# Kernel optimization log

Hardware: AMD Instinct MI355X
Metric: run time of the kernel (lower is better)

The kernel has to match this reference:

```python
import jax, jax.numpy as jnp
import numpy as np

N_NODES = 500_000
N_EDGES = 16_000_000
N_LAYERS = 49
ALPHA = 0.3  # GCN2Conv alpha; beta = 1.0 (no theta/layer given)

# per-layer activation applied AFTER the conv (layer index 0-based)
_LEAKY = {1, 11, 21, 31, 41}
_SIG = {4, 14, 24, 34, 44}


def setup_inputs() -> dict:
    key = jax.random.key(0)
    k1, k2, k3 = jax.random.split(key, 3)
    x = jax.random.normal(k1, (N_NODES, 1), dtype=jnp.float32)
    adj = jax.random.randint(k2, (2, N_EDGES), 0, N_NODES, dtype=jnp.int64)
    # 49 scalar (1x1) layer weights
    w = jax.random.normal(k3, (N_LAYERS,), dtype=jnp.float32) * 0.1
    return {"input": x, "w": w, "adj": adj}


def _gcn_norm(adj, n):
    # add self-loops, symmetric normalization D^-1/2 (A+I) D^-1/2
    loops = jnp.arange(n, dtype=adj.dtype)
    src = jnp.concatenate([adj[0], loops])
    dst = jnp.concatenate([adj[1], loops])
    deg = jax.ops.segment_sum(jnp.ones(src.shape[0], jnp.float32), dst, num_segments=n)
    dis = 1.0 / jnp.sqrt(deg)  # deg >= 1 due to self-loops
    ew = dis[src] * dis[dst]
    return src, dst, ew


def reference(input, w, adj):
    n = input.shape[0]
    x0 = input.astype(jnp.float32)
    src, dst, ew = _gcn_norm(adj, n)
    ewc = ew[:, None]  # [E+N, 1]

    def gcn2(x, wl):
        h = jax.ops.segment_sum(ewc * x[src], dst, num_segments=n)  # A_hat @ x
        comb = (1.0 - ALPHA) * h + ALPHA * x0                       # residual mix
        return comb * wl                                            # 1x1 weight, beta=1

    x = x0
    for i in range(N_LAYERS):
        y = gcn2(x, w[i])
        if i == 0:
            x = y  # no activation after gcn1
        elif i == N_LAYERS - 1:
            x = n * jax.nn.sigmoid(y)  # CustomSigmoid: len(x) * sigmoid(x)
        elif i in _LEAKY:
            x = jax.nn.leaky_relu(y, 0.01)
        elif i in _SIG:
            x = jax.nn.sigmoid(y)
        else:
            x = jax.nn.relu(y)
        # dropout(p=0.0) is identity
    return jnp.squeeze(x, 1).astype(jnp.int64)
```

## Files before the change

kernel.cpp:

```cpp
#include <hip/hip_runtime.h>
#include <math.h>

#define NN 500000
#define NE 16000000
#define NBKT 1954
#define PB 16384
#define NPB_BLOCKS ((NE + PB - 1) / PB)
#define BKT_CAP 9216

__global__ __launch_bounds__(256) void hist_kernel(const int4* __restrict__ dst4,
                                                   int* __restrict__ bcnt) {
    __shared__ int lh[NBKT];
    for (int i = threadIdx.x; i < NBKT; i += 256) lh[i] = 0;
    __syncthreads();
    long base4 = (long)blockIdx.x * (PB / 4);
    for (int k = 0; k < PB / 4; k += 256) {
        long i4 = base4 + k + threadIdx.x;
        if (i4 < NE / 4) {
            int4 d = dst4[i4];
            atomicAdd(&lh[d.x >> 8], 1);
            atomicAdd(&lh[d.y >> 8], 1);
            atomicAdd(&lh[d.z >> 8], 1);
            atomicAdd(&lh[d.w >> 8], 1);
        }
    }
    __syncthreads();
    for (int i = threadIdx.x; i < NBKT; i += 256) {
        int c = lh[i];
        if (c) atomicAdd(&bcnt[i], c);
    }
}

__global__ __launch_bounds__(256) void scan_buckets(int* __restrict__ bcnt,
                                                    int* __restrict__ bbase) {
    __shared__ int sh[256];
    __shared__ int carry_sh;
    if (threadIdx.x == 0) carry_sh = 0;
    __syncthreads();
    for (int base = 0; base < NBKT; base += 256) {
        int i = base + threadIdx.x;
        int v = (i < NBKT) ? bcnt[i] : 0;
        sh[threadIdx.x] = v;
        __syncthreads();
        for (int off = 1; off < 256; off <<= 1) {
            int t = (threadIdx.x >= off) ? sh[threadIdx.x - off] : 0;
            __syncthreads();
            sh[threadIdx.x] += t;
            __syncthreads();
        }
        int incl = sh[threadIdx.x];
        int c = carry_sh;
        __syncthreads();
        if (i < NBKT) {
            int ex = c + incl - v;
            bbase[i] = ex;
            bcnt[i] = ex;
        }
        if (threadIdx.x == 255) carry_sh = c + incl;
        __syncthreads();
    }
    if (threadIdx.x == 0) bbase[NBKT] = NE;
}

__global__ __launch_bounds__(256) void partition_kernel(const int* __restrict__ src,
                                                        const int* __restrict__ dst,
                                                        int* __restrict__ bcur,
                                                        int* __restrict__ ebuf) {
    __shared__ int lh[NBKT];
    for (int i = threadIdx.x; i < NBKT; i += 256) lh[i] = 0;
    __syncthreads();
    long base = (long)blockIdx.x * PB;
    for (int k = 0; k < PB; k += 256) {
        long e = base + k + threadIdx.x;
        if (e < NE) atomicAdd(&lh[dst[e] >> 8], 1);
    }
    __syncthreads();
    for (int i = threadIdx.x; i < NBKT; i += 256) {
        int c = lh[i];
        if (c) lh[i] = atomicAdd(&bcur[i], c);
    }
    __syncthreads();
    for (int k = 0; k < PB; k += 256) {
        long e = base + k + threadIdx.x;
        if (e < NE) {
            int d = dst[e];
            int pos = atomicAdd(&lh[d >> 8], 1);
            ebuf[pos] = ((d & 255) << 19) | src[e];
        }
    }
}

__global__ __launch_bounds__(256) void bucket_csr(const int* __restrict__ bbase,
                                                  int* __restrict__ ebuf,
                                                  int* __restrict__ rp,
                                                  float* __restrict__ dis) {
    __shared__ int eds[BKT_CAP];
    __shared__ int cnt[256];
    __shared__ int scn[256];
    int b = blockIdx.x;
    int ebase = bbase[b];
    int nb = bbase[b + 1] - ebase;
    if (nb > BKT_CAP) nb = BKT_CAP;
    for (int i = threadIdx.x; i < nb; i += 256) eds[i] = ebuf[ebase + i];
    cnt[threadIdx.x] = 0;
    __syncthreads();
    for (int i = threadIdx.x; i < nb; i += 256) atomicAdd(&cnt[eds[i] >> 19], 1);
    __syncthreads();
    int my = cnt[threadIdx.x];
    scn[threadIdx.x] = my;
    __syncthreads();
    for (int off = 1; off < 256; off <<= 1) {
        int t = (threadIdx.x >= off) ? scn[threadIdx.x - off] : 0;
        __syncthreads();
        scn[threadIdx.x] += t;
        __syncthreads();
    }
    int excl = scn[threadIdx.x] - my;
    int v = b * 256 + threadIdx.x;
    if (v < NN) {
        rp[v] = ebase + excl;
        dis[v] = rsqrtf((float)(my + 1));
    }
    __syncthreads();
    cnt[threadIdx.x] = excl;
    __syncthreads();
    for (int i = threadIdx.x; i < nb; i += 256) {
        int p = eds[i];
        int pos = atomicAdd(&cnt[p >> 19], 1);
        ebuf[ebase + pos] = p & 0x7FFFF;
    }
    if (b == 0 && threadIdx.x == 0) rp[NN] = NE;
}

__global__ void init_z(const float* __restrict__ x0, const float* __restrict__ dis,
                       float* __restrict__ z) {
    int i = blockIdx.x * 256 + threadIdx.x;
    if (i < NN) z[i] = x0[i] * dis[i];
}

__global__ __launch_bounds__(256) void layer_kernel(
        const int* __restrict__ rp, const int* __restrict__ csr,
        const float* __restrict__ zin, const float* __restrict__ dis,
        const float* __restrict__ x0, const float* __restrict__ w,
        int li, int act, float* __restrict__ zout, int* __restrict__ out) {
    int tid = blockIdx.x * 256 + threadIdx.x;
    int v = tid >> 3;
    int lane = threadIdx.x & 7;
    int beg = rp[v];
    int end = rp[v + 1];
    float s = 0.f;
    for (int j = beg + lane; j < end; j += 8) s += zin[csr[j]];
    s += __shfl_xor(s, 1);
    s += __shfl_xor(s, 2);
    s += __shfl_xor(s, 4);
    if (lane != 0) return;
    s += zin[v];
    float h = dis[v] * s;
    float comb = 0.7f * h + 0.3f * x0[v];
    float y = comb * w[li];
    if (act == 4) {
        float sg = 1.f / (1.f + expf(-y));
        out[v] = (int)(500000.f * sg);
        return;
    }
    float r;
    if (act == 0)      r = y;
    else if (act == 1) r = fmaxf(y, 0.f);
    else if (act == 2) r = (y > 0.f) ? y : 0.01f * y;
    else               r = 1.f / (1.f + expf(-y));
    zout[v] = dis[v] * r;
}

extern "C" void kernel_launch(void* const* d_in, const int* in_sizes, int n_in,
                              void* d_out, int out_size, void* d_ws, size_t ws_size,
                              hipStream_t stream) {
    const float* x0  = (const float*)d_in[0];
    const float* w   = (const float*)d_in[1];
    const int*   adj = (const int*)d_in[2];
    const int*   src = adj;
    const int*   dst = adj + NE;
    int* out = (int*)d_out;

    uintptr_t p = (uintptr_t)d_ws;
    auto alloc = [&](size_t bytes) -> void* {
        p = (p + 255) & ~(uintptr_t)255;
        void* r = (void*)p;
        p += bytes;
        return r;
    };
    float* dis   = (float*)alloc((size_t)NN * 4);
    int*   rp    = (int*)alloc((size_t)(NN + 1) * 4);
    float* z0    = (float*)alloc((size_t)NN * 4);
    float* z1    = (float*)alloc((size_t)NN * 4);
    int*   bcnt  = (int*)alloc((size_t)NBKT * 4);
    int*   bbase = (int*)alloc((size_t)(NBKT + 1) * 4);
    int*   csr   = (int*)alloc((size_t)NE * 4);
    (void)ws_size;

    hipMemsetAsync(bcnt, 0, (size_t)NBKT * 4, stream);

    hist_kernel<<<NPB_BLOCKS, 256, 0, stream>>>((const int4*)dst, bcnt);
    scan_buckets<<<1, 256, 0, stream>>>(bcnt, bbase);
    partition_kernel<<<NPB_BLOCKS, 256, 0, stream>>>(src, dst, bcnt, csr);
    bucket_csr<<<NBKT, 256, 0, stream>>>(bbase, csr, rp, dis);
    init_z<<<(NN + 255) / 256, 256, 0, stream>>>(x0, dis, z0);

    float* zbuf[2] = {z0, z1};
    const int LB = (NN * 8) / 256;
    for (int i = 0; i < 49; i++) {
        int act;
        if (i == 0)            act = 0;
        else if (i == 48)      act = 4;
        else if (i % 10 == 1)  act = 2;
        else if (i % 10 == 4)  act = 3;
        else                   act = 1;
        layer_kernel<<<LB, 256, 0, stream>>>(rp, csr, zbuf[i & 1], dis, x0, w,
                                             i, act, zbuf[(i + 1) & 1], out);
    }
}
```

Baseline: 4.487 ms.

## Replace per-node CSR with bucketed edge lists and LDS atomic aggregation

The sort stage that turned destination buckets into a full CSR is dropped. Each layer now processes one 256-node bucket per block, reading packed (local dst, src) edges and accumulating into a shared-memory array with float atomics. A smaller kernel computes only the degrees. This removes the in-bucket sort pass and the row-pointer array, and lets edge reads be contiguous per block. The cost is LDS atomic contention in every layer and a float summation order that is no longer deterministic. The partition block size is also enlarged.

```diff
diff --git a/kernel.cpp b/kernel.cpp
--- a/kernel.cpp
+++ b/kernel.cpp
@@ -4,9 +4,8 @@
 #define NN 500000
 #define NE 16000000
 #define NBKT 1954
-#define PB 16384
+#define PB 40960
 #define NPB_BLOCKS ((NE + PB - 1) / PB)
-#define BKT_CAP 9216
 
 __global__ __launch_bounds__(256) void hist_kernel(const int4* __restrict__ dst4,
                                                    int* __restrict__ bcnt) {
@@ -90,46 +89,20 @@
     }
 }
 
-__global__ __launch_bounds__(256) void bucket_csr(const int* __restrict__ bbase,
-                                                  int* __restrict__ ebuf,
-                                                  int* __restrict__ rp,
+__global__ __launch_bounds__(256) void bucket_deg(const int* __restrict__ bbase,
+                                                  const int* __restrict__ ebuf,
                                                   float* __restrict__ dis) {
-    __shared__ int eds[BKT_CAP];
     __shared__ int cnt[256];
-    __shared__ int scn[256];
     int b = blockIdx.x;
     int ebase = bbase[b];
     int nb = bbase[b + 1] - ebase;
-    if (nb > BKT_CAP) nb = BKT_CAP;
-    for (int i = threadIdx.x; i < nb; i += 256) eds[i] = ebuf[ebase + i];
     cnt[threadIdx.x] = 0;
     __syncthreads();
-    for (int i = threadIdx.x; i < nb; i += 256) atomicAdd(&cnt[eds[i] >> 19], 1);
+    for (int i = threadIdx.x; i < nb; i += 256)
+        atomicAdd(&cnt[ebuf[ebase + i] >> 19], 1);
     __syncthreads();
-    int my = cnt[threadIdx.x];
-    scn[threadIdx.x] = my;
-    __syncthreads();
-    for (int off = 1; off < 256; off <<= 1) {
-        int t = (threadIdx.x >= off) ? scn[threadIdx.x - off] : 0;
-        __syncthreads();
-        scn[threadIdx.x] += t;
-        __syncthreads();
-    }
-    int excl = scn[threadIdx.x] - my;
     int v = b * 256 + threadIdx.x;
-    if (v < NN) {
-        rp[v] = ebase + excl;
-        dis[v] = rsqrtf((float)(my + 1));
-    }
-    __syncthreads();
-    cnt[threadIdx.x] = excl;
-    __syncthreads();
-    for (int i = threadIdx.x; i < nb; i += 256) {
-        int p = eds[i];
-        int pos = atomicAdd(&cnt[p >> 19], 1);
-        ebuf[ebase + pos] = p & 0x7FFFF;
-    }
-    if (b == 0 && threadIdx.x == 0) rp[NN] = NE;
+    if (v < NN) dis[v] = rsqrtf((float)(cnt[threadIdx.x] + 1));
 }
 
 __global__ void init_z(const float* __restrict__ x0, const float* __restrict__ dis,
@@ -139,24 +112,26 @@
 }
 
 __global__ __launch_bounds__(256) void layer_kernel(
-        const int* __restrict__ rp, const int* __restrict__ csr,
+        const int* __restrict__ bbase, const int* __restrict__ ebuf,
         const float* __restrict__ zin, const float* __restrict__ dis,
         const float* __restrict__ x0, const float* __restrict__ w,
         int li, int act, float* __restrict__ zout, int* __restrict__ out) {
-    int tid = blockIdx.x * 256 + threadIdx.x;
-    int v = tid >> 3;
-    int lane = threadIdx.x & 7;
-    int beg = rp[v];
-    int end = rp[v + 1];
-    float s = 0.f;
-    for (int j = beg + lane; j < end; j += 8) s += zin[csr[j]];
-    s += __shfl_xor(s, 1);
-    s += __shfl_xor(s, 2);
-    s += __shfl_xor(s, 4);
-    if (lane != 0) return;
-    s += zin[v];
-    float h = dis[v] * s;
-    float comb = 0.7f * h + 0.3f * x0[v];
+    __shared__ float h[256];
+    int b = blockIdx.x;
+    int ebase = bbase[b];
+    int nb = bbase[b + 1] - ebase;
+    h[threadIdx.x] = 0.f;
+    __syncthreads();
+    for (int i = threadIdx.x; i < nb; i += 256) {
+        int e = ebuf[ebase + i];
+        atomicAdd(&h[e >> 19], zin[e & 0x7FFFF]);
+    }
+    __syncthreads();
+    int v = b * 256 + threadIdx.x;
+    if (v >= NN) return;
+    float s = h[threadIdx.x] + zin[v];
+    float hh = dis[v] * s;
+    float comb = 0.7f * hh + 0.3f * x0[v];
     float y = comb * w[li];
     if (act == 4) {
         float sg = 1.f / (1.f + expf(-y));
@@ -189,7 +164,6 @@
         return r;
     };
     float* dis   = (float*)alloc((size_t)NN * 4);
-    int*   rp    = (int*)alloc((size_t)(NN + 1) * 4);
     float* z0    = (float*)alloc((size_t)NN * 4);
     float* z1    = (float*)alloc((size_t)NN * 4);
     int*   bcnt  = (int*)alloc((size_t)NBKT * 4);
@@ -202,11 +176,10 @@
     hist_kernel<<<NPB_BLOCKS, 256, 0, stream>>>((const int4*)dst, bcnt);
     scan_buckets<<<1, 256, 0, stream>>>(bcnt, bbase);
     partition_kernel<<<NPB_BLOCKS, 256, 0, stream>>>(src, dst, bcnt, csr);
-    bucket_csr<<<NBKT, 256, 0, stream>>>(bbase, csr, rp, dis);
+    bucket_deg<<<NBKT, 256, 0, stream>>>(bbase, csr, dis);
     init_z<<<(NN + 255) / 256, 256, 0, stream>>>(x0, dis, z0);
 
     float* zbuf[2] = {z0, z1};
-    const int LB = (NN * 8) / 256;
     for (int i = 0; i < 49; i++) {
         int act;
         if (i == 0)            act = 0;
@@ -214,7 +187,7 @@
         else if (i % 10 == 1)  act = 2;
         else if (i % 10 == 4)  act = 3;
         else                   act = 1;
-        layer_kernel<<<LB, 256, 0, stream>>>(rp, csr, zbuf[i & 1], dis, x0, w,
-                                             i, act, zbuf[(i + 1) & 1], out);
+        layer_kernel<<<NBKT, 256, 0, stream>>>(bbase, csr, zbuf[i & 1], dis, x0, w,
+                                               i, act, zbuf[(i + 1) & 1], out);
     }
 }
```

Result: slower. 4.941 ms (+10.1%).
